# Kernel optimization log

Measured on AMD Instinct MI355X. Metric: run time of the kernel, lower is better.

The kernel has to match this reference:

```python
import jax, jax.numpy as jnp
import numpy as np

N, D, H, E = 8192, 1024, 4096, 8


def setup_inputs() -> dict:
    key = jax.random.key(0)
    ks = jax.random.split(key, 7)
    s_d = 1.0 / np.sqrt(D)
    s_h = 1.0 / np.sqrt(H)
    return {
        "x": jax.random.normal(ks[0], (N, D), dtype=jnp.float32),
        "gate_w": jax.random.uniform(ks[1], (E, D), jnp.float32, -s_d, s_d),
        "gate_b": jax.random.uniform(ks[2], (E,), jnp.float32, -s_d, s_d),
        "w1": jax.random.uniform(ks[3], (E, D, H), jnp.float32, -s_d, s_d),
        "b1": jax.random.uniform(ks[4], (E, H), jnp.float32, -s_d, s_d),
        "w2": jax.random.uniform(ks[5], (E, H, D), jnp.float32, -s_h, s_h),
        "b2": jax.random.uniform(ks[6], (E, D), jnp.float32, -s_h, s_h),
    }


def reference(x, gate_w, gate_b, w1, b1, w2, b2):
    # gate softmax over experts: [N, E]
    gates = jax.nn.softmax(x @ gate_w.T + gate_b, axis=-1)
    # all experts in one batched GEMM pair
    h = jax.nn.relu(jnp.einsum("nd,edh->neh", x, w1) + b1)      # [N, E, H]
    expert_out = jnp.einsum("neh,ehd->ned", h, w2) + b2          # [N, E, D]
    # gated weighted sum over experts
    return jnp.einsum("ne,ned->nd", gates, expert_out)
```

## Files before the change

### kernel.cpp

```cpp
#include <hip/hip_runtime.h>
#include <hip/hip_bf16.h>

typedef _Float16 half8 __attribute__((ext_vector_type(8)));
typedef _Float16 half4v __attribute__((ext_vector_type(4)));
typedef float floatx4 __attribute__((ext_vector_type(4)));

__device__ inline void gload_lds16(const void* g, void* l) {
  __builtin_amdgcn_global_load_lds(
      (const __attribute__((address_space(1))) unsigned int*)g,
      (__attribute__((address_space(3))) unsigned int*)l, 16, 0, 0);
}
__device__ inline unsigned lds_off(const void* p) {
  return (unsigned)(uintptr_t)(const __attribute__((address_space(3))) char*)p;
}
__device__ inline half8 ds_read128(unsigned off) {
  half8 r;
  asm volatile("ds_read_b128 %0, %1" : "=v"(r) : "v"(off));
  return r;
}
#define BARB()   __builtin_amdgcn_s_barrier()
#define WAITL0() asm volatile("s_waitcnt lgkmcnt(0)")
#define WAITV(n) asm volatile("s_waitcnt vmcnt(" #n ")")
#define SCHED0() __builtin_amdgcn_sched_barrier(0)

__device__ inline void xcd_chunk_decode(int* mb, int* nk) {
  if (gridDim.y & 7) { *mb = blockIdx.x; *nk = blockIdx.y; return; }
  const int gx = gridDim.x;
  const int nb = gx * gridDim.y;
  const int b = blockIdx.x + gx * blockIdx.y;
  const int s = (b & 7) * (nb >> 3) + (b >> 3);
  const int PW = gx * 8;
  const int p = s / PW, r = s % PW;
  *mb = r >> 3;
  *nk = p * 8 + (r & 7);
}

__global__ __launch_bounds__(256) void gates_kernel(
    const float* __restrict__ x, const float* __restrict__ gw,
    const float* __restrict__ gb, float* __restrict__ gates) {
  const int lane = threadIdx.x & 63, wid = threadIdx.x >> 6;
  const int n = blockIdx.x * 4 + wid;
  const float* xr = x + (size_t)n * 1024;
  float xv[16];
#pragma unroll
  for (int i = 0; i < 16; ++i) xv[i] = xr[lane + i * 64];
  float logit[8];
#pragma unroll
  for (int e = 0; e < 8; ++e) {
    const float* wr = gw + (size_t)e * 1024;
    float p = 0.f;
#pragma unroll
    for (int i = 0; i < 16; ++i) p += xv[i] * wr[lane + i * 64];
#pragma unroll
    for (int off = 32; off > 0; off >>= 1) p += __shfl_xor(p, off);
    logit[e] = p + gb[e];
  }
  float mx = logit[0];
#pragma unroll
  for (int e = 1; e < 8; ++e) mx = fmaxf(mx, logit[e]);
  float s = 0.f;
#pragma unroll
  for (int e = 0; e < 8; ++e) { logit[e] = expf(logit[e] - mx); s += logit[e]; }
  if (lane < 8) gates[(size_t)n * 8 + lane] = logit[lane] / s;
}

__global__ __launch_bounds__(256) void combine_kernel(
    const float* __restrict__ gates, const float* __restrict__ b2,
    const _Float16* __restrict__ p1, const _Float16* __restrict__ p2,
    float* __restrict__ out) {
  const int i = blockIdx.x * 256 + threadIdx.x;
  const int n = i >> 7;
  const int d0 = (i & 127) << 3;
  const half8 a = *(const half8*)(p1 + ((size_t)n * 1024 + d0));
  const half8 b = *(const half8*)(p2 + ((size_t)n * 1024 + d0));
  float s[8];
#pragma unroll
  for (int j = 0; j < 8; ++j) s[j] = (float)a[j] + (float)b[j];
  const float* g = gates + (size_t)n * 8;
#pragma unroll
  for (int e = 0; e < 8; ++e) {
    const float ge = g[e];
    const float4* bb = (const float4*)(b2 + (size_t)e * 1024 + d0);
    const float4 b0 = bb[0], b1v = bb[1];
    s[0] += ge * b0.x; s[1] += ge * b0.y; s[2] += ge * b0.z; s[3] += ge * b0.w;
    s[4] += ge * b1v.x; s[5] += ge * b1v.y; s[6] += ge * b1v.z; s[7] += ge * b1v.w;
  }
  float4* o = (float4*)(out + (size_t)n * 1024 + d0);
  o[0] = make_float4(s[0], s[1], s[2], s[3]);
  o[1] = make_float4(s[4], s[5], s[6], s[7]);
}

__global__ __launch_bounds__(256) void cvt_f32_f16_kernel(
    const float* __restrict__ in, _Float16* __restrict__ out, int n8) {
  const int i = blockIdx.x * 256 + threadIdx.x;
  if (i >= n8) return;
  const float4* p = (const float4*)(in + (size_t)i * 8);
  float4 a = p[0], b = p[1];
  half8 h;
  h[0] = (_Float16)a.x; h[1] = (_Float16)a.y; h[2] = (_Float16)a.z; h[3] = (_Float16)a.w;
  h[4] = (_Float16)b.x; h[5] = (_Float16)b.y; h[6] = (_Float16)b.z; h[7] = (_Float16)b.w;
  *(half8*)(out + (size_t)i * 8) = h;
}

__global__ __launch_bounds__(256) void transpose_cvt_kernel(
    const float* __restrict__ in, _Float16* __restrict__ out, int R, int C) {
  __shared__ _Float16 tile[32][36];
  const float* src = in + (size_t)blockIdx.z * R * C;
  _Float16* dst = out + (size_t)blockIdx.z * R * C;
  const int c0 = blockIdx.x << 5, r0 = blockIdx.y << 5;
  const int lr = threadIdx.x >> 3, lc = (threadIdx.x & 7) << 2;
  const float4 v = *(const float4*)&src[(size_t)(r0 + lr) * C + c0 + lc];
  half4v h;
  h[0] = (_Float16)v.x; h[1] = (_Float16)v.y;
  h[2] = (_Float16)v.z; h[3] = (_Float16)v.w;
  *(half4v*)&tile[lr][lc] = h;
  __syncthreads();
  const int oc = threadIdx.x >> 3, orr = (threadIdx.x & 7) << 2;
  half4v o;
#pragma unroll
  for (int i = 0; i < 4; ++i) o[i] = tile[orr + i][oc];
  *(half4v*)&dst[(size_t)(c0 + oc) * R + r0 + orr] = o;
}

template <int EPI>
__global__ __launch_bounds__(512, 2) void gemm256_kernel(
    const _Float16* __restrict__ A, const _Float16* __restrict__ Bt,
    const float* __restrict__ bias, const float* __restrict__ gates,
    int ebase, _Float16* __restrict__ Hout, _Float16* __restrict__ p1,
    _Float16* __restrict__ p2, int beta, int kOff, int lda, int ldb,
    int kLen, int Nout) {
  __shared__ _Float16 smem[2][4][8192];
  const int tid = threadIdx.x, lane = tid & 63, wid = tid >> 6;
  const int wm = wid >> 2, wn = wid & 3;

  int mb, nk;
  xcd_chunk_decode(&mb, &nk);
  const int m0 = mb * 256;
  int n0, kb = 0, q = 0;
  if (EPI == 1) { q = nk >> 2; n0 = (nk & 3) * 256; kb = q * kOff; }
  else          { n0 = nk * 256; }
  const int eg = (EPI == 0) ? ebase + (n0 >> 12) : 0;
  const int NT = kLen >> 6;

  floatx4 acc[8][4] = {};

  auto stage_half = [&](int h) {
    if (h >= 4 * NT) return;
    const int th = h >> 2, j = h & 3, bf = th & 1;
    const int k0 = kb + th * 64;
    const char* gb; int ld, rorig;
    if (j < 2) { gb = (const char*)A;  ld = lda; rorig = m0 + j * 128; }
    else       { gb = (const char*)Bt; ld = ldb; rorig = n0 + (j - 2) * 128; }
    _Float16* lb = &smem[bf][j][0];
#pragma unroll
    for (int i = 0; i < 2; ++i) {
      const int row = (wid * 2 + i) * 8 + (lane >> 3);
      const int gkb = ((lane & 7) * 16) ^ ((row & 7) << 4);
      gload_lds16(gb + ((size_t)(rorig + row) * ld + k0) * 2 + gkb,
                  lb + (wid * 2 + i) * 512 + lane * 8);
    }
  };

  const unsigned smem0 = lds_off(&smem[0][0][0]);
  auto ldA = [&](int bf, int mf, int ks) -> half8 {
    const int row = mf * 16 + (lane & 15);
    const int col = (ks * 64 + ((lane >> 4) << 4)) ^ ((row & 7) << 4);
    return ds_read128(smem0 + (bf * 4 + wm) * 16384 + row * 128 + col);
  };
  auto ldB = [&](int bf, int nf, int ks) -> half8 {
    const int c = wn * 64 + nf * 16 + (lane & 15);
    const int r = c & 127;
    const int col = (ks * 64 + ((lane >> 4) << 4)) ^ ((r & 7) << 4);
    return ds_read128(smem0 + (bf * 4 + 2 + (c >> 7)) * 16384 + r * 128 + col);
  };

  stage_half(0); stage_half(1); stage_half(2); stage_half(3);
  stage_half(4 * 1 + 2); stage_half(4 * 1 + 3);
  WAITV(4); SCHED0();
  BARB();

#pragma unroll 1
  for (int t = 0; t < NT; ++t) {
    const int bf = t & 1;
    half8 a[4][2], bh[2][2], bl[2][2];
#pragma unroll
    for (int ks = 0; ks < 2; ++ks) {
#pragma unroll
      for (int m = 0; m < 4; ++m) a[m][ks] = ldA(bf, m, ks);
#pragma unroll
      for (int n = 0; n < 2; ++n) bh[n][ks] = ldB(bf, 2 + n, ks);
    }
    stage_half(4 * (t + 1) + 0);
    BARB(); WAITL0(); SCHED0();
    __builtin_amdgcn_s_setprio(1);
#pragma unroll
    for (int m = 0; m < 4; ++m)
#pragma unroll
      for (int n = 0; n < 2; ++n)
#pragma unroll
        for (int ks = 0; ks < 2; ++ks)
          acc[m][2 + n] = __builtin_amdgcn_mfma_f32_16x16x32_f16(
              a[m][ks], bh[n][ks], acc[m][2 + n], 0, 0, 0);
    __builtin_amdgcn_s_setprio(0);
    BARB();
#pragma unroll
    for (int ks = 0; ks < 2; ++ks)
#pragma unroll
      for (int n = 0; n < 2; ++n) bl[n][ks] = ldB(bf, n, ks);
    stage_half(4 * (t + 1) + 1);
    BARB(); WAITL0(); SCHED0();
    __builtin_amdgcn_s_setprio(1);
#pragma unroll
    for (int m = 0; m < 4; ++m)
#pragma unroll
      for (int n = 0; n < 2; ++n)
#pragma unroll
        for (int ks = 0; ks < 2; ++ks)
          acc[m][n] = __builtin_amdgcn_mfma_f32_16x16x32_f16(
              a[m][ks], bl[n][ks], acc[m][n], 0, 0, 0);
    __builtin_amdgcn_s_setprio(0);
    BARB();
#pragma unroll
    for (int ks = 0; ks < 2; ++ks)
#pragma unroll
      for (int m = 0; m < 4; ++m) a[m][ks] = ldA(bf, 4 + m, ks);
    stage_half(4 * (t + 2) + 2);
    BARB(); WAITL0(); SCHED0();
    __builtin_amdgcn_s_setprio(1);
#pragma unroll
    for (int m = 0; m < 4; ++m)
#pragma unroll
      for (int n = 0; n < 2; ++n)
#pragma unroll
        for (int ks = 0; ks < 2; ++ks)
          acc[4 + m][2 + n] = __builtin_amdgcn_mfma_f32_16x16x32_f16(
              a[m][ks], bh[n][ks], acc[4 + m][2 + n], 0, 0, 0);
    __builtin_amdgcn_s_setprio(0);
    BARB();
    stage_half(4 * (t + 2) + 3);
    BARB();
    __builtin_amdgcn_s_setprio(1);
#pragma unroll
    for (int m = 0; m < 4; ++m)
#pragma unroll
      for (int n = 0; n < 2; ++n)
#pragma unroll
        for (int ks = 0; ks < 2; ++ks)
          acc[4 + m][n] = __builtin_amdgcn_mfma_f32_16x16x32_f16(
              a[m][ks], bl[n][ks], acc[4 + m][n], 0, 0, 0);
    __builtin_amdgcn_s_setprio(0);
    if (t + 2 < NT) { WAITV(4); } else { WAITV(0); }
    SCHED0();
    BARB();
  }

#pragma unroll
  for (int mf = 0; mf < 8; ++mf) {
    const int gr0 = m0 + wm * 128 + mf * 16 + ((lane >> 4) << 2);
#pragma unroll
    for (int r = 0; r < 4; ++r) {
      const int gr = gr0 + r;
      float g = 0.f;
      if (EPI == 0) g = gates[(size_t)gr * 8 + eg];
#pragma unroll
      for (int nf = 0; nf < 4; ++nf) {
        const int gc = n0 + wn * 64 + nf * 16 + (lane & 15);
        if (EPI == 0) {
          const float v = acc[mf][nf][r] + bias[gc];
          Hout[(size_t)gr * Nout + gc] = (_Float16)(g * fmaxf(v, 0.0f));
        } else {
          _Float16* P = (q ? p2 : p1) + (size_t)gr * Nout + gc;
          if (beta) *P = (_Float16)((float)*P + acc[mf][nf][r]);
          else      *P = (_Float16)acc[mf][nf][r];
        }
      }
    }
  }
}

extern "C" void kernel_launch(void* const* d_in, const int* in_sizes, int n_in,
                              void* d_out, int out_size, void* d_ws,
                              size_t ws_size, hipStream_t stream) {
  const float* x  = (const float*)d_in[0];
  const float* gw = (const float*)d_in[1];
  const float* gb = (const float*)d_in[2];
  const float* w1 = (const float*)d_in[3];
  const float* b1 = (const float*)d_in[4];
  const float* w2 = (const float*)d_in[5];
  const float* b2 = (const float*)d_in[6];
  float* out = (float*)d_out;

  const int N = 8192, D = 1024, H = 4096, E = 8;
  const size_t MB = 1ull << 20;

  char* ws = (char*)d_ws;
  float* gates  = (float*)ws;
  _Float16* x_h = (_Float16*)(ws + MB);

  gates_kernel<<<N / 4, 256, 0, stream>>>(x, gw, gb, gates);
  cvt_f32_f16_kernel<<<(N * D / 8 + 255) / 256, 256, 0, stream>>>(x, x_h, N * D / 8);

  if (ws_size >= 210 * MB) {
    _Float16* Hbuf2 = (_Float16*)(ws + 17 * MB);
    _Float16* w2tp  = (_Float16*)(ws + 145 * MB);
    _Float16* w1tp  = (_Float16*)(ws + 161 * MB);
    _Float16* p1    = (_Float16*)(ws + 177 * MB);
    _Float16* p2    = (_Float16*)(ws + 193 * MB);
    for (int p = 0; p < 4; ++p) {
      transpose_cvt_kernel<<<dim3(H / 32, D / 32, 2), 256, 0, stream>>>(
          w1 + (size_t)(2 * p) * D * H, w1tp, D, H);
      transpose_cvt_kernel<<<dim3(D / 32, 2 * H / 32, 1), 256, 0, stream>>>(
          w2 + (size_t)(2 * p) * H * D, w2tp, 2 * H, D);
      gemm256_kernel<0><<<dim3(N / 256, 2 * H / 256), 512, 0, stream>>>(
          x_h, w1tp, b1 + (size_t)(2 * p) * H, gates, 2 * p, Hbuf2,
          nullptr, nullptr, 0, 0, D, D, D, 2 * H);
      gemm256_kernel<1><<<dim3(N / 256, 8), 512, 0, stream>>>(
          Hbuf2, w2tp, nullptr, nullptr, 0, nullptr, p1, p2, p > 0, H,
          2 * H, 2 * H, H, D);
    }
    combine_kernel<<<N * D / 8 / 256, 256, 0, stream>>>(gates, b2, p1, p2, out);
  } else if (ws_size >= 186 * MB) {
    _Float16* Hbuf = (_Float16*)(ws + 17 * MB);
    _Float16* w2t  = (_Float16*)(ws + 81 * MB);
    _Float16* w1t  = (_Float16*)(ws + 145 * MB);
    _Float16* p1   = (_Float16*)(ws + 153 * MB);
    _Float16* p2   = (_Float16*)(ws + 169 * MB);
    transpose_cvt_kernel<<<dim3(D / 32, H / 32, E), 256, 0, stream>>>(
        w2, w2t, H, D);
    for (int e = 0; e < E; ++e) {
      transpose_cvt_kernel<<<dim3(H / 32, D / 32, 1), 256, 0, stream>>>(
          w1 + (size_t)e * D * H, w1t, D, H);
      gemm256_kernel<0><<<dim3(N / 256, H / 256), 512, 0, stream>>>(
          x_h, w1t, b1 + (size_t)e * H, gates, e, Hbuf, nullptr, nullptr, 0,
          0, D, D, D, H);
      gemm256_kernel<1><<<dim3(N / 256, 8), 512, 0, stream>>>(
          Hbuf, w2t + (size_t)e * D * H, nullptr, nullptr, 0, nullptr,
          p1, p2, e > 0, H / 2, H, H, H / 2, D);
    }
    combine_kernel<<<N * D / 8 / 256, 256, 0, stream>>>(gates, b2, p1, p2, out);
  } else {
    _Float16* w1t  = (_Float16*)(ws + 17 * MB);
    _Float16* w2t  = (_Float16*)(ws + 25 * MB);
    _Float16* Hbuf = (_Float16*)(ws + 33 * MB);
    _Float16* p1   = (_Float16*)(ws + 97 * MB);
    _Float16* p2   = (_Float16*)(ws + 113 * MB);
    for (int e = 0; e < E; ++e) {
      transpose_cvt_kernel<<<dim3(H / 32, D / 32, 1), 256, 0, stream>>>(
          w1 + (size_t)e * D * H, w1t, D, H);
      transpose_cvt_kernel<<<dim3(D / 32, H / 32, 1), 256, 0, stream>>>(
          w2 + (size_t)e * H * D, w2t, H, D);
      gemm256_kernel<0><<<dim3(N / 256, H / 256), 512, 0, stream>>>(
          x_h, w1t, b1 + (size_t)e * H, gates, e, Hbuf, nullptr, nullptr, 0,
          0, D, D, D, H);
      gemm256_kernel<1><<<dim3(N / 256, 8), 512, 0, stream>>>(
          Hbuf, w2t, nullptr, nullptr, 0, nullptr, p1, p2, e > 0, H / 2,
          H, H, H / 2, D);
    }
    combine_kernel<<<N * D / 8 / 256, 256, 0, stream>>>(gates, b2, p1, p2, out);
  }
}
```

Before: 1.256 ms.

## Batch weight transposes up front and store per-pair partials for one final combine

When the workspace is large enough, all w1 and w2 weights are transposed and converted in two launches before the GEMM loop, replacing eight smaller per-pair transpose launches. Each pair's second GEMM now writes its two partial outputs to separate buffers without accumulating into earlier results. A new combine kernel then sums all eight fp16 partials with the gated biases. This removes the read-modify-write of the partial buffers across pairs and the serialized transpose launches, at the cost of much more workspace and a heavier final combine that reads eight partial arrays.

```diff
diff --git a/kernel.cpp b/kernel.cpp
--- a/kernel.cpp
+++ b/kernel.cpp
@@ -76,6 +76,35 @@
   float s[8];
 #pragma unroll
   for (int j = 0; j < 8; ++j) s[j] = (float)a[j] + (float)b[j];
+  const float* g = gates + (size_t)n * 8;
+#pragma unroll
+  for (int e = 0; e < 8; ++e) {
+    const float ge = g[e];
+    const float4* bb = (const float4*)(b2 + (size_t)e * 1024 + d0);
+    const float4 b0 = bb[0], b1v = bb[1];
+    s[0] += ge * b0.x; s[1] += ge * b0.y; s[2] += ge * b0.z; s[3] += ge * b0.w;
+    s[4] += ge * b1v.x; s[5] += ge * b1v.y; s[6] += ge * b1v.z; s[7] += ge * b1v.w;
+  }
+  float4* o = (float4*)(out + (size_t)n * 1024 + d0);
+  o[0] = make_float4(s[0], s[1], s[2], s[3]);
+  o[1] = make_float4(s[4], s[5], s[6], s[7]);
+}
+
+__global__ __launch_bounds__(256) void combine8_kernel(
+    const float* __restrict__ gates, const float* __restrict__ b2,
+    const _Float16* __restrict__ pAll, float* __restrict__ out) {
+  const int i = blockIdx.x * 256 + threadIdx.x;
+  const int n = i >> 7;
+  const int d0 = (i & 127) << 3;
+  const size_t off = (size_t)n * 1024 + d0;
+  const size_t stride = (size_t)8192 * 1024;
+  float s[8] = {0, 0, 0, 0, 0, 0, 0, 0};
+#pragma unroll
+  for (int pi = 0; pi < 8; ++pi) {
+    const half8 a = *(const half8*)(pAll + pi * stride + off);
+#pragma unroll
+    for (int j = 0; j < 8; ++j) s[j] += (float)a[j];
+  }
   const float* g = gates + (size_t)n * 8;
 #pragma unroll
   for (int e = 0; e < 8; ++e) {
@@ -300,7 +329,27 @@
   gates_kernel<<<N / 4, 256, 0, stream>>>(x, gw, gb, gates);
   cvt_f32_f16_kernel<<<(N * D / 8 + 255) / 256, 256, 0, stream>>>(x, x_h, N * D / 8);
 
-  if (ws_size >= 210 * MB) {
+  if (ws_size >= 402 * MB) {
+    _Float16* Hbuf2 = (_Float16*)(ws + 17 * MB);
+    _Float16* w1t   = (_Float16*)(ws + 145 * MB);
+    _Float16* w2tp  = (_Float16*)(ws + 209 * MB);
+    _Float16* pAll  = (_Float16*)(ws + 273 * MB);
+    transpose_cvt_kernel<<<dim3(H / 32, D / 32, E), 256, 0, stream>>>(
+        w1, w1t, D, H);
+    transpose_cvt_kernel<<<dim3(D / 32, 2 * H / 32, 4), 256, 0, stream>>>(
+        w2, w2tp, 2 * H, D);
+    const size_t ND = (size_t)N * D;
+    for (int p = 0; p < 4; ++p) {
+      gemm256_kernel<0><<<dim3(N / 256, 2 * H / 256), 512, 0, stream>>>(
+          x_h, w1t + (size_t)(2 * p) * H * D, b1 + (size_t)(2 * p) * H, gates,
+          2 * p, Hbuf2, nullptr, nullptr, 0, 0, D, D, D, 2 * H);
+      gemm256_kernel<1><<<dim3(N / 256, 8), 512, 0, stream>>>(
+          Hbuf2, w2tp + (size_t)p * D * 2 * H, nullptr, nullptr, 0, nullptr,
+          pAll + (size_t)(2 * p) * ND, pAll + (size_t)(2 * p + 1) * ND, 0, H,
+          2 * H, 2 * H, H, D);
+    }
+    combine8_kernel<<<N * D / 8 / 256, 256, 0, stream>>>(gates, b2, pAll, out);
+  } else if (ws_size >= 210 * MB) {
     _Float16* Hbuf2 = (_Float16*)(ws + 17 * MB);
     _Float16* w2tp  = (_Float16*)(ws + 145 * MB);
     _Float16* w1tp  = (_Float16*)(ws + 161 * MB);
```

New measurement: 1.186 ms. 1.06x faster.
